# Kernel tuning notes

Measured on AMD Instinct MI355X. Metric: run time of the kernel, lower is better.

## Reference

```python
import jax, jax.numpy as jnp
import numpy as np

# dims derived from init_kwargs
N_NODES = 100000            # type_mask.shape[0]
N0, N1 = 60000, 40000       # nodes per type
F0, F1 = 128, 64            # feats_dim_list
HID = 64                    # hidden_dim (= in_dim of layer1)
HEADS = 8
OUT = 16
ATTN_VEC = 128
E = 250000                  # metapath instances per metapath
L = 3                       # nodes per metapath instance (2 edge types)
NG = 8192                   # nodes in each minibatch DGL graph
B = 8192                    # number of target nodes
ETYPES = [[0, 1], [2, 3]]   # etypes_list; num_edge_type=4, RotatE0 -> 2 base relations


def setup_inputs() -> dict:
    ks = jax.random.split(jax.random.key(0), 20)
    g = lambda k, s, sc=1.0: sc * jax.random.normal(k, s, dtype=jnp.float32)
    return {
        "feat0": g(ks[0], (N0, F0)),
        "feat1": g(ks[1], (N1, F1)),
        "W0": g(ks[2], (HID, F0), 0.12),
        "b0": jnp.zeros((HID,), jnp.float32),
        "W1": g(ks[3], (HID, F1), 0.15),
        "b1": jnp.zeros((HID,), jnp.float32),
        "r_vec": g(ks[4], (2, HID // 2, 2), 0.2),
        "attn0": g(ks[5], (HEADS, HID), 0.2),
        "attn1": g(ks[6], (HEADS, HID), 0.2),
        "fc1_w": g(ks[7], (ATTN_VEC, HEADS * HID), 0.06),
        "fc1_b": jnp.zeros((ATTN_VEC,), jnp.float32),
        "fc2_w": g(ks[8], (1, ATTN_VEC), 0.1),
        "fc_w": g(ks[9], (OUT, HEADS * HID), 0.06),
        "fc_b": jnp.zeros((OUT,), jnp.float32),
        "idx0": jnp.arange(N0, dtype=jnp.int32),                 # type-0 node ids (contiguous block)
        "idx1": jnp.arange(N1, dtype=jnp.int32) + N0,            # type-1 node ids (offset block)
        "mp0_indices": jax.random.randint(ks[10], (E, L), 0, N_NODES, dtype=jnp.int32),
        "mp0_dst": jax.random.randint(ks[11], (E,), 0, NG, dtype=jnp.int32),
        "mp0_target": jax.random.randint(ks[12], (B,), 0, NG, dtype=jnp.int32),
        "mp1_indices": jax.random.randint(ks[13], (E, L), 0, N_NODES, dtype=jnp.int32),
        "mp1_dst": jax.random.randint(ks[14], (E,), 0, NG, dtype=jnp.int32),
        "mp1_target": jax.random.randint(ks[15], (B,), 0, NG, dtype=jnp.int32),
    }


def _cmul(a, b):
    # complex multiply on trailing dim of size 2
    re = a[..., 0] * b[..., 0] - a[..., 1] * b[..., 1]
    im = a[..., 0] * b[..., 1] + a[..., 1] * b[..., 0]
    return jnp.stack([re, im], axis=-1)


def reference(feat0, feat1, W0, b0, W1, b1, r_vec, attn0, attn1,
              fc1_w, fc1_b, fc2_w, fc_w, fc_b,
              idx0, idx1,
              mp0_indices, mp0_dst, mp0_target,
              mp1_indices, mp1_dst, mp1_target):
    # per-node-type linear scattered into a dense [N, HID] table (dropout=0 / eval)
    tf = jnp.zeros((N_NODES, HID), jnp.float32)
    tf = tf.at[idx0].set(feat0 @ W0.T + b0)
    tf = tf.at[idx1].set(feat1 @ W1.T + b1)

    # RotatE0: unit-modulus normalize, then double relations with conjugates
    rv = r_vec / jnp.linalg.norm(r_vec, axis=-1, keepdims=True)          # [2, HID//2, 2]
    conj = rv * jnp.array([1.0, -1.0], rv.dtype)
    rv_full = jnp.stack([rv, conj], axis=1).reshape(-1, HID // 2, 2)     # [4, HID//2, 2]

    def metapath(indices, dst, target, attn, etypes):
        edata = tf[indices].reshape(E, L, HID // 2, 2)   # gather metapath instances
        # suffix products of rotations: final[i] = prod_{j>=i} r[etypes[j]], final[L-1]=1
        final = [jnp.stack([jnp.ones(HID // 2, jnp.float32),
                            jnp.zeros(HID // 2, jnp.float32)], -1)]
        for i in range(L - 2, -1, -1):
            final.insert(0, _cmul(final[0], rv_full[etypes[i]]))
        finals = jnp.stack(final, axis=0)                # [L, HID//2, 2]
        edata = _cmul(edata, finals)                     # rotate every path position
        h = edata.reshape(E, L, HID).mean(axis=1)        # [E, HID] instance encoding
        # node-level attention (heads share h: torch tiles hidden across heads)
        a = jax.nn.leaky_relu(h @ attn.T, 0.01)          # [E, HEADS]
        m = jax.ops.segment_max(a, dst, num_segments=NG)
        ex = jnp.exp(a - m[dst])
        s = jax.ops.segment_sum(ex, dst, num_segments=NG)
        an = ex / s[dst]                                 # edge softmax per destination
        eft = jnp.einsum('eh,ed->ehd', an, h)            # [E, HEADS, HID]
        ft = jax.ops.segment_sum(eft, dst, num_segments=NG)
        ret = ft[target].reshape(B, HEADS * HID)
        return jax.nn.elu(ret)

    out0 = metapath(mp0_indices, mp0_dst, mp0_target, attn0, ETYPES[0])
    out1 = metapath(mp1_indices, mp1_dst, mp1_target, attn1, ETYPES[1])

    # metapath-level attention
    outs = jnp.stack([out0, out1], axis=0)               # [P, B, HEADS*HID]
    s1 = jnp.tanh(outs @ fc1_w.T + fc1_b)                # [P, B, ATTN_VEC]
    beta = jax.nn.softmax((s1.mean(axis=1) @ fc2_w.T)[:, 0], axis=0)  # [P]
    hagg = jnp.einsum('p,pbf->bf', beta, outs)           # [B, HEADS*HID]
    logits = hagg @ fc_w.T + fc_b                        # [B, OUT]
    return logits, hagg
```

## Files before the change

### kernel.cpp

```cpp
#include <hip/hip_runtime.h>
#include <hip/hip_fp16.h>
#include <math.h>

#define NNODES 100000
#define NT0 60000
#define NT1 40000
#define FD0 128
#define FD1 64
#define HID 64
#define HEADS 8
#define OUTD 16
#define AVEC 128
#define NE 250000
#define NG 8192
#define NB 8192

typedef _Float16 half8v __attribute__((ext_vector_type(8)));
typedef float f32x4 __attribute__((ext_vector_type(4)));

#define OFF_TF16    0ull
#define OFF_FINALS  3200000ull
#define OFF_ACC     3200512ull
#define OFF_BETA    3200768ull
#define OFF_WC0     3201024ull
#define OFF_WC1     3208192ull
#define OFF_BC0     3211776ull
#define OFF_BC1     3211904ull
#define OFF_FC1H    3212032ull
#define OFF_P       3244800ull
#define OFF_SORTED  5644800ull
#define OFF_COUNTS  7644800ull
#define OFF_CNTT    7661184ull
#define OFF_CURS    7677568ull
#define OFF_OFFS    7693952ull
#define OFF_FT16    7710592ull

__device__ __forceinline__ float2 rot_pair(const float* r_vec, int pi, int j){
  const float2* rv = (const float2*)r_vec;
  int rel = pi >= 3 ? 1 : 0;
  float2 r = rv[rel*32 + j];
  float n = rsqrtf(r.x*r.x + r.y*r.y);
  r.x *= n; r.y *= n;
  float2 rf = make_float2(r.x, -r.y);
  int pos = pi - rel*3;
  if (pos == 2) return make_float2(1.f, 0.f);
  if (pos == 1) return rf;
  return make_float2(rf.x*r.x - rf.y*r.y, rf.x*r.y + rf.y*r.x);
}

__global__ void k_prep0(const float* __restrict__ r_vec, float* __restrict__ finals,
                        float* __restrict__ acc, float* __restrict__ beta){
  int t = threadIdx.x;
  if (t < 32){
    float2* F = (float2*)finals;
    #pragma unroll
    for (int pi = 0; pi < 6; ++pi) F[pi*32 + t] = rot_pair(r_vec, pi, t);
  }
  for (int q = t; q < 256; q += 64) acc[q] = 0.f;
  if (t < 2) beta[t] = 0.f;
}

__global__ __launch_bounds__(128) void k_wcat(const float* __restrict__ r_vec,
     const float* __restrict__ attn0, const float* __restrict__ attn1,
     const float* __restrict__ W0v, const float* __restrict__ b0v,
     const float* __restrict__ W1v, const float* __restrict__ b1v,
     const float* __restrict__ fc1_w,
     __half* __restrict__ wc0, float* __restrict__ bc0,
     __half* __restrict__ wc1, float* __restrict__ bc1,
     __half* __restrict__ fc1h){
  int bid = blockIdx.x;
  int t = threadIdx.x;
  if (bid >= 224){
    int base = (bid - 224)*1024;
    for (int i = t; i < 1024; i += 128)
      fc1h[base + i] = __float2half(fc1_w[base + i]);
    return;
  }
  int type = bid >= 112;
  int c = bid - type*112;
  int F = type ? FD1 : FD0;
  const float* W  = type ? W1v : W0v;
  const float* bv = type ? b1v : b0v;
  __half* wc = type ? wc1 : wc0;
  float* bc  = type ? bc1 : bc0;

  if (c < 64){
    for (int f = t; f < F; f += 128) wc[(size_t)c*F + f] = __float2half(W[(size_t)c*F + f]);
    if (t == 0) bc[c] = bv[c];
    return;
  }
  __shared__ float a[64];
  int cg = c - 64;
  int pi = cg >> 3, k = cg & 7;
  if (t < 32){
    float2 f = rot_pair(r_vec, pi, t);
    const float* at = (pi >= 3) ? attn1 : attn0;
    float a0 = at[k*64 + 2*t], a1 = at[k*64 + 2*t + 1];
    a[2*t]     = (f.x*a0 + f.y*a1) * (1.f/3.f);
    a[2*t + 1] = (f.x*a1 - f.y*a0) * (1.f/3.f);
  }
  __syncthreads();
  for (int f = t; f < F; f += 128){
    float s = 0.f;
    #pragma unroll 16
    for (int d = 0; d < 64; ++d) s += a[d] * W[(size_t)d*F + f];
    wc[(size_t)c*F + f] = __float2half(s);
  }
  if (t == 0){
    float s = 0.f;
    #pragma unroll 16
    for (int d = 0; d < 64; ++d) s += a[d] * bv[d];
    bc[c] = s;
  }
}

__global__ __launch_bounds__(256) void k_tform(const float* __restrict__ feat0,
      const int* __restrict__ idx0, const float* __restrict__ feat1,
      const int* __restrict__ idx1,
      const __half* __restrict__ wc0, const float* __restrict__ bc0,
      const __half* __restrict__ wc1, const float* __restrict__ bc1,
      __half* __restrict__ tf16, __half* __restrict__ P){
  const int nb0 = (NT0 + 63)/64;
  int bid = blockIdx.x;
  const float* feat; const int* idx; const __half* wc; const float* bc;
  int n_nodes, F, m0;
  if (bid < nb0){ feat=feat0; idx=idx0; wc=wc0; bc=bc0; n_nodes=NT0; F=FD0; m0=bid*64; }
  else { feat=feat1; idx=idx1; wc=wc1; bc=bc1; n_nodes=NT1; F=FD1; m0=(bid-nb0)*64; }
  __shared__ int idxs[64];
  int t = threadIdx.x;
  if (t < 64){
    int gm = m0 + t; if (gm > n_nodes - 1) gm = n_nodes - 1;
    idxs[t] = idx[gm];
  }
  __syncthreads();
  int w = t >> 6, l = t & 63;
  int lr = l & 15, lk = l >> 4;
  int gr = m0 + w*16 + lr; if (gr > n_nodes - 1) gr = n_nodes - 1;
  const float* arow = feat + (size_t)gr*F;

  f32x4 acc7[7];
  #pragma unroll
  for (int ct = 0; ct < 7; ++ct) acc7[ct] = (f32x4){0.f,0.f,0.f,0.f};

  int nk = F >> 5;
  for (int kk = 0; kk < nk; ++kk){
    int koff = kk*32 + lk*8;
    float4 ua = *(const float4*)(arow + koff);
    float4 ub = *(const float4*)(arow + koff + 4);
    half8v a = {(_Float16)ua.x,(_Float16)ua.y,(_Float16)ua.z,(_Float16)ua.w,
                (_Float16)ub.x,(_Float16)ub.y,(_Float16)ub.z,(_Float16)ub.w};
    #pragma unroll
    for (int ct = 0; ct < 7; ++ct){
      half8v b = *(const half8v*)(wc + (size_t)(ct*16 + lr)*F + koff);
      acc7[ct] = __builtin_amdgcn_mfma_f32_16x16x32_f16(a, b, acc7[ct], 0, 0, 0);
    }
  }

  #pragma unroll
  for (int ct = 0; ct < 7; ++ct){
    int col = ct*16 + lr;
    float bvv = bc[col];
    #pragma unroll
    for (int r = 0; r < 4; ++r){
      int nl = w*16 + lk*4 + r;
      int gm = m0 + nl;
      if (gm < n_nodes){
        __half hv = __float2half(acc7[ct][r] + bvv);
        int gn = idxs[nl];
        if (col < 64) tf16[(size_t)gn*64 + col] = hv;
        else {
          int cg = col - 64;
          int p = cg >= 24;
          P[(size_t)p*2400000 + (size_t)gn*24 + (cg - p*24)] = hv;
        }
      }
    }
  }
}

__global__ void k_zeroi(int* __restrict__ p, int n){
  int t = blockIdx.x*blockDim.x + threadIdx.x;
  if (t < n) p[t] = 0;
}

__global__ void k_hist3(const int* __restrict__ d0, const int* __restrict__ d1,
                        const int* __restrict__ t0, const int* __restrict__ t1,
                        int* __restrict__ counts, int* __restrict__ cntt){
  int e = blockIdx.x*blockDim.x + threadIdx.x;
  if (e < NE) atomicAdd(&counts[d0[e]], 1);
  else if (e < 2*NE) atomicAdd(&counts[NG + d1[e-NE]], 1);
  else if (e < 2*NE + NB) atomicAdd(&cntt[t0[e-2*NE]], 1);
  else if (e < 2*NE + 2*NB) atomicAdd(&cntt[NG + t1[e-2*NE-NB]], 1);
}

__global__ __launch_bounds__(1024) void k_scan(const int* __restrict__ counts,
                                               int* __restrict__ offs,
                                               int* __restrict__ curs){
  __shared__ int lds[1024];
  int t = threadIdx.x;
  int base = t*16;
  int v[16]; int sum = 0;
  #pragma unroll
  for (int i = 0; i < 16; ++i){ v[i] = counts[base+i]; sum += v[i]; }
  lds[t] = sum;
  __syncthreads();
  for (int off = 1; off < 1024; off <<= 1){
    int x = (t >= off) ? lds[t-off] : 0;
    __syncthreads();
    lds[t] += x;
    __syncthreads();
  }
  int excl = lds[t] - sum;
  #pragma unroll
  for (int i = 0; i < 16; ++i){ offs[base+i] = excl; excl += v[i]; curs[base+i] = 0; }
  if (t == 1023) offs[2*NG] = excl;
}

__global__ void k_scatter2(const int* __restrict__ m0, const int* __restrict__ d0,
                           const int* __restrict__ m1, const int* __restrict__ d1,
                           const int* __restrict__ offs, int* __restrict__ curs,
                           int4* __restrict__ sorted){
  int e = blockIdx.x*blockDim.x + threadIdx.x;
  if (e >= 2*NE) return;
  const int* mp; int d;
  if (e < NE){ mp = m0 + (size_t)e*3; d = d0[e]; }
  else { mp = m1 + (size_t)(e-NE)*3; d = NG + d1[e-NE]; }
  int pos = offs[d] + atomicAdd(&curs[d], 1);
  sorted[pos] = make_int4(mp[0], mp[1], mp[2], 0);
}

__global__ __launch_bounds__(64) void k_seg(const __half* __restrict__ tf16,
                                            const __half* __restrict__ P,
                                            const int4* __restrict__ sorted,
                                            const int* __restrict__ offs,
                                            const float* __restrict__ finals,
                                            __half* __restrict__ ft16o){
  int bid = blockIdx.x;
  int p = bid >> 13;
  int lane = threadIdx.x;
  int hw = lane >> 5, j = lane & 31;
  int start = offs[bid], end = offs[bid+1];
  __half2* ftw = (__half2*)(ft16o + (size_t)bid*512);
  if (start == end){
    #pragma unroll
    for (int kk = 0; kk < 4; ++kk) ftw[(hw*4+kk)*32 + j] = __floats2half2_rn(0.f, 0.f);
    return;
  }
  const float2* F2 = (const float2*)(finals + p*192);
  float2 f0 = F2[j], f1 = F2[32 + j];
  const __half2* tfh = (const __half2*)tf16;
  const __half* Pp = P + (size_t)p*2400000;

  __shared__ int4 ndb[64];
  __shared__ float wb[64][8];

  float sA[8], ur[8], ui[8];
  #pragma unroll
  for (int k = 0; k < 8; ++k){ sA[k] = 0.f; ur[k] = 0.f; ui[k] = 0.f; }

  for (int c = start; c < end; c += 64){
    int n = end - c; if (n > 64) n = 64;
    if (lane < n){
      int4 nd = sorted[c + lane];
      ndb[lane] = nd;
      float4 rA = *(const float4*)(Pp + (size_t)nd.x*24);
      float4 rB = *(const float4*)(Pp + (size_t)nd.y*24 + 8);
      float4 rC = *(const float4*)(Pp + (size_t)nd.z*24 + 16);
      const __half2* ha = (const __half2*)&rA;
      const __half2* hb = (const __half2*)&rB;
      const __half2* hc = (const __half2*)&rC;
      float w[8];
      #pragma unroll
      for (int m = 0; m < 4; ++m){
        float2 va = __half22float2(ha[m]);
        float2 vb = __half22float2(hb[m]);
        float2 vc = __half22float2(hc[m]);
        float x0 = va.x + vb.x + vc.x;
        float x1 = va.y + vb.y + vc.y;
        x0 = x0 > 0.f ? x0 : 0.01f*x0;
        x1 = x1 > 0.f ? x1 : 0.01f*x1;
        w[2*m]   = __expf(x0);
        w[2*m+1] = __expf(x1);
      }
      #pragma unroll
      for (int k = 0; k < 8; ++k) sA[k] += w[k];
      *(float4*)&wb[lane][0] = make_float4(w[0], w[1], w[2], w[3]);
      *(float4*)&wb[lane][4] = make_float4(w[4], w[5], w[6], w[7]);
    }
    __syncthreads();
    int cend = c + n;
    for (int i = c + hw; i < cend; i += 2){
      int e = i - c;
      int4 nd = ndb[e];
      float4 wlo = *(const float4*)&wb[e][0];
      float4 whi = *(const float4*)&wb[e][4];
      float2 v0 = __half22float2(tfh[(size_t)nd.x*32 + j]);
      float2 v1 = __half22float2(tfh[(size_t)nd.y*32 + j]);
      float2 v2 = __half22float2(tfh[(size_t)nd.z*32 + j]);
      float hre = (v0.x*f0.x - v0.y*f0.y) + (v1.x*f1.x - v1.y*f1.y) + v2.x;
      float him = (v0.x*f0.y + v0.y*f0.x) + (v1.x*f1.y + v1.y*f1.x) + v2.y;
      ur[0] += wlo.x*hre; ui[0] += wlo.x*him;
      ur[1] += wlo.y*hre; ui[1] += wlo.y*him;
      ur[2] += wlo.z*hre; ui[2] += wlo.z*him;
      ur[3] += wlo.w*hre; ui[3] += wlo.w*him;
      ur[4] += whi.x*hre; ui[4] += whi.x*him;
      ur[5] += whi.y*hre; ui[5] += whi.y*him;
      ur[6] += whi.z*hre; ui[6] += whi.z*him;
      ur[7] += whi.w*hre; ui[7] += whi.w*him;
    }
    __syncthreads();
  }
  #pragma unroll
  for (int k = 0; k < 8; ++k){
    ur[k] += __shfl_xor(ur[k], 32);
    ui[k] += __shfl_xor(ui[k], 32);
    float v = sA[k];
    #pragma unroll
    for (int mask = 1; mask < 64; mask <<= 1) v += __shfl_xor(v, mask);
    sA[k] = v;
  }
  #pragma unroll
  for (int kk = 0; kk < 4; ++kk){
    int k = hw*4 + kk;
    float inv = 1.f / (3.f * sA[k]);
    float re = ur[k]*inv, im = ui[k]*inv;
    re = re > 0.f ? re : expm1f(re);
    im = im > 0.f ? im : expm1f(im);
    ftw[k*32 + j] = __floats2half2_rn(re, im);
  }
}

__global__ __launch_bounds__(256) void k_s1g(const __half* __restrict__ ft16o,
                                             const int* __restrict__ cntt,
                                             const __half* __restrict__ fc1h,
                                             const float* __restrict__ fc1_b,
                                             float* __restrict__ acc_p){
  int bid = blockIdx.x;
  int p  = bid >> 8;
  int rb = bid & 255;
  int t = threadIdx.x;
  int w = t >> 6, l = t & 63;
  int rowbase = rb*32 + (w & 1)*16;
  int colbase = (w >> 1)*64;
  int lr = l & 15, lk = l >> 4;

  const half8v* Ab = (const half8v*)(ft16o + ((size_t)p*NG + rowbase)*512);
  f32x4 acc[4] = {{0.f,0.f,0.f,0.f},{0.f,0.f,0.f,0.f},
                  {0.f,0.f,0.f,0.f},{0.f,0.f,0.f,0.f}};

  #pragma unroll 4
  for (int kk = 0; kk < 16; ++kk){
    half8v a = Ab[(size_t)lr*64 + kk*4 + lk];
    #pragma unroll
    for (int ct = 0; ct < 4; ++ct){
      const half8v* Bb = (const half8v*)(fc1h + (size_t)(colbase + ct*16 + lr)*512);
      half8v b = Bb[kk*4 + lk];
      acc[ct] = __builtin_amdgcn_mfma_f32_16x16x32_f16(a, b, acc[ct], 0, 0, 0);
    }
  }

  float cf[4];
  #pragma unroll
  for (int r = 0; r < 4; ++r)
    cf[r] = (float)cntt[p*NG + rowbase + lk*4 + r];
  #pragma unroll
  for (int ct = 0; ct < 4; ++ct){
    int col = colbase + ct*16 + lr;
    float bv = fc1_b[col];
    float sv = 0.f;
    #pragma unroll
    for (int r = 0; r < 4; ++r)
      sv += cf[r] * tanhf(acc[ct][r] + bv);
    sv += __shfl_xor(sv, 16);
    sv += __shfl_xor(sv, 32);
    if (l < 16) atomicAdd(&acc_p[p*128 + col], sv);
  }
}

__global__ void k_beta(const float* __restrict__ acc, const float* __restrict__ fc2_w,
                       float* __restrict__ beta){
  int t = threadIdx.x;
  float s0 = acc[t]*fc2_w[t] + acc[t+64]*fc2_w[t+64];
  float s1 = acc[128+t]*fc2_w[t] + acc[192+t]*fc2_w[t+64];
  #pragma unroll
  for (int mask = 1; mask < 64; mask <<= 1){
    s0 += __shfl_xor(s0, mask, 64);
    s1 += __shfl_xor(s1, mask, 64);
  }
  if (t == 0){
    float z0 = s0 / (float)NB, z1 = s1 / (float)NB;
    float mz = fmaxf(z0, z1);
    float e0 = expf(z0 - mz), e1 = expf(z1 - mz);
    float inv = 1.f / (e0 + e1);
    beta[0] = e0*inv; beta[1] = e1*inv;
  }
}

__global__ void k_final(const __half* __restrict__ ft0, const __half* __restrict__ ft1,
                        const int* __restrict__ tgt0, const int* __restrict__ tgt1,
                        const float* __restrict__ beta, const float* __restrict__ fc_w,
                        const float* __restrict__ fc_b, float* __restrict__ d_out){
  __shared__ float lds[512];
  int b = blockIdx.x, t = threadIdx.x;
  float b0 = beta[0], b1 = beta[1];
  int g0 = tgt0[b], g1 = tgt1[b];
  float v0 = __half2float(ft0[(size_t)g0*512 + t]);
  float v1 = __half2float(ft1[(size_t)g1*512 + t]);
  float h = b0*v0 + b1*v1;
  lds[t] = h;
  d_out[(size_t)NB*OUTD + (size_t)b*512 + t] = h;
  __syncthreads();
  int o = t >> 5, j = t & 31;
  float s = 0.f;
  const float* w = fc_w + o*512;
  for (int d = j; d < 512; d += 32) s += lds[d]*w[d];
  #pragma unroll
  for (int mask = 1; mask < 32; mask <<= 1) s += __shfl_xor(s, mask, 32);
  if (j == 0) d_out[(size_t)b*OUTD + o] = s + fc_b[o];
}

extern "C" void kernel_launch(void* const* d_in, const int* in_sizes, int n_in,
                              void* d_out, int out_size, void* d_ws, size_t ws_size,
                              hipStream_t stream){
  const float* feat0  = (const float*)d_in[0];
  const float* feat1  = (const float*)d_in[1];
  const float* W0     = (const float*)d_in[2];
  const float* b0     = (const float*)d_in[3];
  const float* W1     = (const float*)d_in[4];
  const float* b1     = (const float*)d_in[5];
  const float* r_vec  = (const float*)d_in[6];
  const float* attn0  = (const float*)d_in[7];
  const float* attn1  = (const float*)d_in[8];
  const float* fc1_w  = (const float*)d_in[9];
  const float* fc1_b  = (const float*)d_in[10];
  const float* fc2_w  = (const float*)d_in[11];
  const float* fc_w   = (const float*)d_in[12];
  const float* fc_b   = (const float*)d_in[13];
  const int*   idx0   = (const int*)d_in[14];
  const int*   idx1   = (const int*)d_in[15];
  const int*   mpi0   = (const int*)d_in[16];
  const int*   mdst0  = (const int*)d_in[17];
  const int*   mtgt0  = (const int*)d_in[18];
  const int*   mpi1   = (const int*)d_in[19];
  const int*   mdst1  = (const int*)d_in[20];
  const int*   mtgt1  = (const int*)d_in[21];

  float* ws      = (float*)d_ws;
  __half* tf16   = (__half*)(ws + OFF_TF16);
  float* finals  = ws + OFF_FINALS;
  float* acc     = ws + OFF_ACC;
  float* beta    = ws + OFF_BETA;
  __half* wc0    = (__half*)(ws + OFF_WC0);
  __half* wc1    = (__half*)(ws + OFF_WC1);
  float* bc0     = ws + OFF_BC0;
  float* bc1     = ws + OFF_BC1;
  __half* fc1h   = (__half*)(ws + OFF_FC1H);
  __half* P      = (__half*)(ws + OFF_P);
  int4*  sorted  = (int4*)(ws + OFF_SORTED);
  int*   counts  = (int*)(ws + OFF_COUNTS);
  int*   cntt    = (int*)(ws + OFF_CNTT);
  int*   curs    = (int*)(ws + OFF_CURS);
  int*   offs    = (int*)(ws + OFF_OFFS);
  __half* ft16o  = (__half*)(ws + OFF_FT16);
  __half* ft0h   = ft16o;
  __half* ft1h   = ft16o + (size_t)NG*512;

  k_prep0<<<1, 64, 0, stream>>>(r_vec, finals, acc, beta);
  k_wcat<<<288, 128, 0, stream>>>(r_vec, attn0, attn1, W0, b0, W1, b1, fc1_w,
                                  wc0, bc0, wc1, bc1, fc1h);
  k_zeroi<<<128, 256, 0, stream>>>(counts, 4*NG);
  k_hist3<<<(2*NE + 2*NB + 255)/256, 256, 0, stream>>>(mdst0, mdst1, mtgt0, mtgt1,
                                                       counts, cntt);
  k_scan<<<1, 1024, 0, stream>>>(counts, offs, curs);
  k_scatter2<<<(2*NE + 255)/256, 256, 0, stream>>>(mpi0, mdst0, mpi1, mdst1,
                                                   offs, curs, sorted);

  k_tform<<<(NT0 + 63)/64 + (NT1 + 63)/64, 256, 0, stream>>>(
      feat0, idx0, feat1, idx1, wc0, bc0, wc1, bc1, tf16, P);

  k_seg<<<2*NG, 64, 0, stream>>>(tf16, P, sorted, offs, finals, ft16o);

  k_s1g<<<512, 256, 0, stream>>>(ft16o, cntt, fc1h, fc1_b, acc);
  k_beta<<<1, 64, 0, stream>>>(acc, fc2_w, beta);
  k_final<<<NB, 512, 0, stream>>>(ft0h, ft1h, mtgt0, mtgt1, beta, fc_w, fc_b,
                                  (float*)d_out);
}
```

Before: 230.4 us.

## Merge prep kernels, stage tform outputs in LDS, pack two segments per seg block

Folds the prep kernel into k_wcat as an extra block and replaces the zeroing kernel with hipMemsetAsync, cutting launch count. k_tform now writes results to shared memory and emits 16-byte vector stores instead of scattered half stores. k_seg processes two destination segments per 128-thread block, one per wavefront, and swaps __syncthreads for wave-local LDS waits. The memset size (2*16384 ints) matches the old 4*NG zeroing. The wave-local sync relies on each wave touching only its own LDS slice.

```diff
diff --git a/kernel.cpp b/kernel.cpp
--- a/kernel.cpp
+++ b/kernel.cpp
@@ -48,18 +48,6 @@
   return make_float2(rf.x*r.x - rf.y*r.y, rf.x*r.y + rf.y*r.x);
 }
 
-__global__ void k_prep0(const float* __restrict__ r_vec, float* __restrict__ finals,
-                        float* __restrict__ acc, float* __restrict__ beta){
-  int t = threadIdx.x;
-  if (t < 32){
-    float2* F = (float2*)finals;
-    #pragma unroll
-    for (int pi = 0; pi < 6; ++pi) F[pi*32 + t] = rot_pair(r_vec, pi, t);
-  }
-  for (int q = t; q < 256; q += 64) acc[q] = 0.f;
-  if (t < 2) beta[t] = 0.f;
-}
-
 __global__ __launch_bounds__(128) void k_wcat(const float* __restrict__ r_vec,
      const float* __restrict__ attn0, const float* __restrict__ attn1,
      const float* __restrict__ W0v, const float* __restrict__ b0v,
@@ -67,9 +55,20 @@
      const float* __restrict__ fc1_w,
      __half* __restrict__ wc0, float* __restrict__ bc0,
      __half* __restrict__ wc1, float* __restrict__ bc1,
-     __half* __restrict__ fc1h){
+     __half* __restrict__ fc1h,
+     float* __restrict__ finals, float* __restrict__ acc, float* __restrict__ beta){
   int bid = blockIdx.x;
   int t = threadIdx.x;
+  if (bid == 288){
+    if (t < 32){
+      float2* F = (float2*)finals;
+      #pragma unroll
+      for (int pi = 0; pi < 6; ++pi) F[pi*32 + t] = rot_pair(r_vec, pi, t);
+    }
+    for (int q = t; q < 256; q += 128) acc[q] = 0.f;
+    if (t < 2) beta[t] = 0.f;
+    return;
+  }
   if (bid >= 224){
     int base = (bid - 224)*1024;
     for (int i = t; i < 1024; i += 128)
@@ -127,6 +126,7 @@
   if (bid < nb0){ feat=feat0; idx=idx0; wc=wc0; bc=bc0; n_nodes=NT0; F=FD0; m0=bid*64; }
   else { feat=feat1; idx=idx1; wc=wc1; bc=bc1; n_nodes=NT1; F=FD1; m0=(bid-nb0)*64; }
   __shared__ int idxs[64];
+  __shared__ __half outs[64][120];
   int t = threadIdx.x;
   if (t < 64){
     int gm = m0 + t; if (gm > n_nodes - 1) gm = n_nodes - 1;
@@ -163,24 +163,27 @@
     #pragma unroll
     for (int r = 0; r < 4; ++r){
       int nl = w*16 + lk*4 + r;
-      int gm = m0 + nl;
-      if (gm < n_nodes){
-        __half hv = __float2half(acc7[ct][r] + bvv);
-        int gn = idxs[nl];
-        if (col < 64) tf16[(size_t)gn*64 + col] = hv;
-        else {
-          int cg = col - 64;
-          int p = cg >= 24;
-          P[(size_t)p*2400000 + (size_t)gn*24 + (cg - p*24)] = hv;
-        }
-      }
-    }
-  }
-}
-
-__global__ void k_zeroi(int* __restrict__ p, int n){
-  int t = blockIdx.x*blockDim.x + threadIdx.x;
-  if (t < n) p[t] = 0;
+      outs[nl][col] = __float2half(acc7[ct][r] + bvv);
+    }
+  }
+  __syncthreads();
+  #pragma unroll
+  for (int u = t; u < 512; u += 256){
+    int n = u >> 3, c = u & 7;
+    if (m0 + n < n_nodes){
+      uint4 v = *(uint4*)&outs[n][c*8];
+      *(uint4*)&tf16[(size_t)idxs[n]*64 + c*8] = v;
+    }
+  }
+  for (int u = t; u < 384; u += 256){
+    int pp = u >= 192;
+    int rr = u - pp*192;
+    int n = rr / 3, c = rr - n*3;
+    if (m0 + n < n_nodes){
+      uint4 v = *(uint4*)&outs[n][64 + pp*24 + c*8];
+      *(uint4*)&P[(size_t)pp*2400000 + (size_t)idxs[n]*24 + c*8] = v;
+    }
+  }
 }
 
 __global__ void k_hist3(const int* __restrict__ d0, const int* __restrict__ d1,
@@ -229,18 +232,21 @@
   sorted[pos] = make_int4(mp[0], mp[1], mp[2], 0);
 }
 
-__global__ __launch_bounds__(64) void k_seg(const __half* __restrict__ tf16,
-                                            const __half* __restrict__ P,
-                                            const int4* __restrict__ sorted,
-                                            const int* __restrict__ offs,
-                                            const float* __restrict__ finals,
-                                            __half* __restrict__ ft16o){
-  int bid = blockIdx.x;
-  int p = bid >> 13;
-  int lane = threadIdx.x;
+__global__ __launch_bounds__(128) void k_seg(const __half* __restrict__ tf16,
+                                             const __half* __restrict__ P,
+                                             const int4* __restrict__ sorted,
+                                             const int* __restrict__ offs,
+                                             const float* __restrict__ finals,
+                                             __half* __restrict__ ft16o){
+  __shared__ int4 ndb[2][64];
+  __shared__ float wb[2][64][8];
+  int wv = threadIdx.x >> 6;
+  int seg = blockIdx.x*2 + wv;
+  int p = seg >> 13;
+  int lane = threadIdx.x & 63;
   int hw = lane >> 5, j = lane & 31;
-  int start = offs[bid], end = offs[bid+1];
-  __half2* ftw = (__half2*)(ft16o + (size_t)bid*512);
+  int start = offs[seg], end = offs[seg+1];
+  __half2* ftw = (__half2*)(ft16o + (size_t)seg*512);
   if (start == end){
     #pragma unroll
     for (int kk = 0; kk < 4; ++kk) ftw[(hw*4+kk)*32 + j] = __floats2half2_rn(0.f, 0.f);
@@ -250,9 +256,8 @@
   float2 f0 = F2[j], f1 = F2[32 + j];
   const __half2* tfh = (const __half2*)tf16;
   const __half* Pp = P + (size_t)p*2400000;
-
-  __shared__ int4 ndb[64];
-  __shared__ float wb[64][8];
+  int4* nb = ndb[wv];
+  float (*wbp)[8] = wb[wv];
 
   float sA[8], ur[8], ui[8];
   #pragma unroll
@@ -262,7 +267,7 @@
     int n = end - c; if (n > 64) n = 64;
     if (lane < n){
       int4 nd = sorted[c + lane];
-      ndb[lane] = nd;
+      nb[lane] = nd;
       float4 rA = *(const float4*)(Pp + (size_t)nd.x*24);
       float4 rB = *(const float4*)(Pp + (size_t)nd.y*24 + 8);
       float4 rC = *(const float4*)(Pp + (size_t)nd.z*24 + 16);
@@ -284,16 +289,17 @@
       }
       #pragma unroll
       for (int k = 0; k < 8; ++k) sA[k] += w[k];
-      *(float4*)&wb[lane][0] = make_float4(w[0], w[1], w[2], w[3]);
-      *(float4*)&wb[lane][4] = make_float4(w[4], w[5], w[6], w[7]);
-    }
-    __syncthreads();
+      *(float4*)&wbp[lane][0] = make_float4(w[0], w[1], w[2], w[3]);
+      *(float4*)&wbp[lane][4] = make_float4(w[4], w[5], w[6], w[7]);
+    }
+    asm volatile("s_waitcnt lgkmcnt(0)" ::: "memory");
+    __builtin_amdgcn_sched_barrier(0);
     int cend = c + n;
     for (int i = c + hw; i < cend; i += 2){
       int e = i - c;
-      int4 nd = ndb[e];
-      float4 wlo = *(const float4*)&wb[e][0];
-      float4 whi = *(const float4*)&wb[e][4];
+      int4 nd = nb[e];
+      float4 wlo = *(const float4*)&wbp[e][0];
+      float4 whi = *(const float4*)&wbp[e][4];
       float2 v0 = __half22float2(tfh[(size_t)nd.x*32 + j]);
       float2 v1 = __half22float2(tfh[(size_t)nd.y*32 + j]);
       float2 v2 = __half22float2(tfh[(size_t)nd.z*32 + j]);
@@ -308,7 +314,8 @@
       ur[6] += whi.z*hre; ui[6] += whi.z*him;
       ur[7] += whi.w*hre; ui[7] += whi.w*him;
     }
-    __syncthreads();
+    asm volatile("s_waitcnt lgkmcnt(0)" ::: "memory");
+    __builtin_amdgcn_sched_barrier(0);
   }
   #pragma unroll
   for (int k = 0; k < 8; ++k){
@@ -465,10 +472,9 @@
   __half* ft0h   = ft16o;
   __half* ft1h   = ft16o + (size_t)NG*512;
 
-  k_prep0<<<1, 64, 0, stream>>>(r_vec, finals, acc, beta);
-  k_wcat<<<288, 128, 0, stream>>>(r_vec, attn0, attn1, W0, b0, W1, b1, fc1_w,
-                                  wc0, bc0, wc1, bc1, fc1h);
-  k_zeroi<<<128, 256, 0, stream>>>(counts, 4*NG);
+  k_wcat<<<289, 128, 0, stream>>>(r_vec, attn0, attn1, W0, b0, W1, b1, fc1_w,
+                                  wc0, bc0, wc1, bc1, fc1h, finals, acc, beta);
+  hipMemsetAsync(counts, 0, 2*16384*sizeof(int), stream);
   k_hist3<<<(2*NE + 2*NB + 255)/256, 256, 0, stream>>>(mdst0, mdst1, mtgt0, mtgt1,
                                                        counts, cntt);
   k_scan<<<1, 1024, 0, stream>>>(counts, offs, curs);
@@ -478,7 +484,7 @@
   k_tform<<<(NT0 + 63)/64 + (NT1 + 63)/64, 256, 0, stream>>>(
       feat0, idx0, feat1, idx1, wc0, bc0, wc1, bc1, tf16, P);
 
-  k_seg<<<2*NG, 64, 0, stream>>>(tf16, P, sorted, offs, finals, ft16o);
+  k_seg<<<NG, 128, 0, stream>>>(tf16, P, sorted, offs, finals, ft16o);
 
   k_s1g<<<512, 256, 0, stream>>>(ft16o, cntt, fc1h, fc1_b, acc);
   k_beta<<<1, 64, 0, stream>>>(acc, fc2_w, beta);
```

Result: faster. 225.6 us (-2.1%).
